# Optimization experiments

Hardware: AMD Instinct MI355X
Metric: run time of the kernel (lower is better)

The kernel has to match this reference:

```python
import jax, jax.numpy as jnp
import numpy as np

E = 8           # num experts
TOPK = 2
NUM_TOKENS = 4096
K = 2048        # hidden dim
N = 2816        # intermediate dim
P = NUM_TOKENS * TOPK   # num_valid_tokens (token, expert-slot) pairs
PE = P // E             # pairs per expert (token-sorted, equal load)


def setup_inputs() -> dict:
    key = jax.random.key(0)
    ks = jax.random.split(key, 6)
    x = jax.random.normal(ks[0], (NUM_TOKENS, K), dtype=jnp.float32)
    W1 = jax.random.normal(ks[1], (E, N, K), dtype=jnp.float32) * (K ** -0.5)  # gate proj
    W3 = jax.random.normal(ks[2], (E, N, K), dtype=jnp.float32) * (K ** -0.5)  # up proj
    W2 = jax.random.normal(ks[3], (E, K, N), dtype=jnp.float32) * (N ** -0.5)  # down proj
    topk_weights = jax.random.uniform(ks[4], (P,), dtype=jnp.float32)          # router weights per pair
    sorted_token_ids = jax.random.randint(ks[5], (P,), 0, NUM_TOKENS, dtype=jnp.int32)
    # token-sorted dispatch: pairs grouped by expert, equal count per expert
    expert_ids = jnp.repeat(jnp.arange(E, dtype=jnp.int32), PE)
    return {"x": x, "W1": W1, "W3": W3, "W2": W2,
            "topk_weights": topk_weights,
            "sorted_token_ids": sorted_token_ids,
            "expert_ids": expert_ids}


def reference(x, W1, W3, W2, topk_weights, sorted_token_ids, expert_ids):
    # Pairs are grouped by expert (token-sorted dispatch), PE pairs per expert.
    eids = expert_ids.reshape(E, PE)[:, 0]            # expert id per group
    xg = x[sorted_token_ids].reshape(E, PE, K)        # gather token activations per pair
    gate = jnp.einsum('epk,enk->epn', xg, W1[eids])   # [E, PE, N]
    up = jnp.einsum('epk,enk->epn', xg, W3[eids])     # [E, PE, N]
    # kernel computes sigmoid(gate) * up (as written in the triton body)
    h = jax.nn.sigmoid(gate) * up
    out_p = jnp.einsum('epn,ekn->epk', h, W2[eids])   # down proj, [E, PE, K]
    out_p = out_p * topk_weights.reshape(E, PE, 1)
    # scatter-add per-pair results into per-token output (atomic_add in kernel)
    out = jnp.zeros((x.shape[0], K), dtype=x.dtype)
    out = out.at[sorted_token_ids].add(out_p.reshape(P, K))
    return out
```

## Files before the change

kernel.cpp:

```cpp
#include <hip/hip_runtime.h>
#include <hip/hip_bf16.h>
#include <cstdint>

typedef __bf16 bf16_t;
typedef __attribute__((ext_vector_type(8))) __bf16 bf16x8;
typedef __attribute__((ext_vector_type(4))) __bf16 bf16x4;
typedef __attribute__((ext_vector_type(4))) float f32x4;

#define NEXP 8
#define NTOK 4096
#define DK   2048
#define DN   2816
#define DN2  5632
#define NP   8192
#define PPE  1024

__global__ void k_convert(const float* __restrict__ src, bf16_t* __restrict__ dst,
                          int perExp4, long dstStride, long dstOff, int total4) {
    int stride = gridDim.x * blockDim.x;
    for (int i = blockIdx.x * blockDim.x + threadIdx.x; i < total4; i += stride) {
        int e  = i / perExp4;
        int r4 = i - e * perExp4;
        float4 v = reinterpret_cast<const float4*>(src)[i];
        bf16x4 o = { (bf16_t)v.x, (bf16_t)v.y, (bf16_t)v.z, (bf16_t)v.w };
        *reinterpret_cast<bf16x4*>(dst + (long)e * dstStride + dstOff + (long)r4 * 4) = o;
    }
}

__global__ void k_gather(const float* __restrict__ x, const int* __restrict__ ids,
                         bf16_t* __restrict__ xg) {
    int i = blockIdx.x * blockDim.x + threadIdx.x;
    if (i >= NP * (DK / 4)) return;
    int p  = i >> 9;
    int c4 = i & 511;
    int tok = ids[p];
    float4 v = reinterpret_cast<const float4*>(x + (size_t)tok * DK)[c4];
    bf16x4 o = { (bf16_t)v.x, (bf16_t)v.y, (bf16_t)v.z, (bf16_t)v.w };
    *reinterpret_cast<bf16x4*>(xg + (size_t)p * DK + c4 * 4) = o;
}

__global__ void k_act(bf16_t* __restrict__ gu) {
    int i = blockIdx.x * blockDim.x + threadIdx.x;
    if (i >= NP * (DN / 8)) return;
    int p = i / (DN / 8);
    int c = i - p * (DN / 8);
    bf16_t* row = gu + (size_t)p * DN2 + c * 8;
    bf16x8 g = *reinterpret_cast<const bf16x8*>(row);
    bf16x8 u = *reinterpret_cast<const bf16x8*>(row + DN);
    bf16x8 h;
#pragma unroll
    for (int j = 0; j < 8; ++j) {
        float gf = (float)g[j], uf = (float)u[j];
        float s = 1.0f / (1.0f + __expf(-gf));
        h[j] = (bf16_t)(s * uf);
    }
    *reinterpret_cast<bf16x8*>(row) = h;
}

__device__ __forceinline__ void gl2lds16(const bf16_t* g, bf16_t* l) {
    __builtin_amdgcn_global_load_lds(
        (__attribute__((address_space(1))) void*)(const_cast<bf16_t*>(g)),
        (__attribute__((address_space(3))) void*)(l), 16, 0, 0);
}

template <int EPI>
__launch_bounds__(256, 2)
__global__ void k_gemm(const bf16_t* __restrict__ A, const bf16_t* __restrict__ B,
                       bf16_t* __restrict__ Cb, float* __restrict__ Cf,
                       const float* __restrict__ tw, const int* __restrict__ ids,
                       int Mtiles, int Ntiles, int Kd, int lda, int ldb,
                       long aStride, long bStride, int ldc, long cStride) {
    __shared__ bf16_t As[128 * 64];
    __shared__ bf16_t Bs[128 * 64];
    const int tpe = Mtiles * Ntiles;
    const int e  = blockIdx.x / tpe;
    const int r  = blockIdx.x - e * tpe;
    const int mt = r / Ntiles;
    const int nt = r - mt * Ntiles;
    const bf16_t* Ae = A + (long)e * aStride + (long)mt * 128 * lda;
    const bf16_t* Be = B + (long)e * bStride + (long)nt * 128 * ldb;
    const int wid  = threadIdx.x >> 6;
    const int lane = threadIdx.x & 63;
    const int wr = wid >> 1, wc = wid & 1;
    const int lr = lane & 15;
    const int lk = (lane >> 4) * 8;
    const int srow = wid * 32 + (lane >> 3);
    const int scol = (lane & 7) * 8;

    f32x4 acc[4][4];
#pragma unroll
    for (int a = 0; a < 4; ++a)
#pragma unroll
        for (int b = 0; b < 4; ++b) acc[a][b] = (f32x4){0.f, 0.f, 0.f, 0.f};

    const int kTiles = Kd >> 6;
    for (int kt = 0; kt < kTiles; ++kt) {
        __syncthreads();
        const bf16_t* ap = Ae + kt * 64 + scol;
        const bf16_t* bp = Be + kt * 64 + scol;
#pragma unroll
        for (int j = 0; j < 4; ++j) {
            gl2lds16(ap + (long)(srow + j * 8) * lda, &As[(wid * 32 + j * 8) * 64]);
            gl2lds16(bp + (long)(srow + j * 8) * ldb, &Bs[(wid * 32 + j * 8) * 64]);
        }
        __syncthreads();
#pragma unroll
        for (int kk = 0; kk < 2; ++kk) {
            bf16x8 af[4], bfr[4];
#pragma unroll
            for (int mi = 0; mi < 4; ++mi)
                af[mi] = *reinterpret_cast<const bf16x8*>(
                    &As[(wr * 64 + mi * 16 + lr) * 64 + kk * 32 + lk]);
#pragma unroll
            for (int ni = 0; ni < 4; ++ni)
                bfr[ni] = *reinterpret_cast<const bf16x8*>(
                    &Bs[(wc * 64 + ni * 16 + lr) * 64 + kk * 32 + lk]);
#pragma unroll
            for (int mi = 0; mi < 4; ++mi)
#pragma unroll
                for (int ni = 0; ni < 4; ++ni)
                    acc[mi][ni] = __builtin_amdgcn_mfma_f32_16x16x32_bf16(
                        af[mi], bfr[ni], acc[mi][ni], 0, 0, 0);
        }
    }

    const int orow0 = wr * 64 + (lane >> 4) * 4;
    const int ocol0 = wc * 64 + (lane & 15);
    if constexpr (EPI == 0) {
        bf16_t* Ce = Cb + (long)e * cStride + (long)mt * 128 * ldc + (long)nt * 128;
#pragma unroll
        for (int mi = 0; mi < 4; ++mi)
#pragma unroll
            for (int i = 0; i < 4; ++i) {
                int row = orow0 + mi * 16 + i;
#pragma unroll
                for (int ni = 0; ni < 4; ++ni)
                    Ce[(long)row * ldc + ocol0 + ni * 16] = (bf16_t)acc[mi][ni][i];
            }
    } else {
        const int p0 = e * PPE + mt * 128;
#pragma unroll
        for (int mi = 0; mi < 4; ++mi)
#pragma unroll
            for (int i = 0; i < 4; ++i) {
                int gp  = p0 + orow0 + mi * 16 + i;
                float w = tw[gp];
                float* orow = Cf + (size_t)ids[gp] * DK + nt * 128 + ocol0;
#pragma unroll
                for (int ni = 0; ni < 4; ++ni)
                    atomicAdd(&orow[ni * 16], acc[mi][ni][i] * w);
            }
    }
}

extern "C" void kernel_launch(void* const* d_in, const int* in_sizes, int n_in,
                              void* d_out, int out_size, void* d_ws, size_t ws_size,
                              hipStream_t stream) {
    const float* x   = (const float*)d_in[0];
    const float* W1  = (const float*)d_in[1];
    const float* W3  = (const float*)d_in[2];
    const float* W2  = (const float*)d_in[3];
    const float* tw  = (const float*)d_in[4];
    const int*   sid = (const int*)d_in[5];
    float* out = (float*)d_out;

    char* ws = (char*)d_ws;
    bf16_t* w13b = (bf16_t*)ws;
    bf16_t* w2b  = (bf16_t*)(ws + 184549376L);
    bf16_t* xg   = (bf16_t*)(ws + 184549376L + 92274688L);
    bf16_t* gu   = (bf16_t*)(ws + 184549376L + 92274688L + 33554432L);

    hipMemsetAsync(d_out, 0, (size_t)out_size * sizeof(float), stream);

    const int per4 = DN * DK / 4;
    const int tot4 = NEXP * per4;
    k_convert<<<2048, 256, 0, stream>>>(W1, w13b, per4, (long)DN2 * DK, 0L, tot4);
    k_convert<<<2048, 256, 0, stream>>>(W3, w13b, per4, (long)DN2 * DK, (long)DN * DK, tot4);
    k_convert<<<2048, 256, 0, stream>>>(W2, w2b, per4, (long)DK * DN, 0L, tot4);
    k_gather<<<NP * (DK / 4) / 256, 256, 0, stream>>>(x, sid, xg);

    k_gemm<0><<<NEXP * 8 * 44, 256, 0, stream>>>(
        xg, w13b, gu, nullptr, nullptr, nullptr,
        8, 44, DK, DK, DK, (long)PPE * DK, (long)DN2 * DK, DN2, (long)PPE * DN2);

    k_act<<<NP * (DN / 8) / 256, 256, 0, stream>>>(gu);

    k_gemm<1><<<NEXP * 8 * 16, 256, 0, stream>>>(
        gu, w2b, nullptr, out, tw, sid,
        8, 16, DN, DN2, DN, (long)PPE * DN2, (long)DK * DN, 0, 0L);
}
```

Baseline: 614.5 us.

## Rewrite MoE GEMMs with 256x256 double-buffered tiles and fused SiLU-style gating epilogue

The GEMM kernel now uses 512-thread blocks with 256x256 tiles, double-buffered LDS with XOR swizzling, interleaved staging and MFMA phases, and setprio hints around the MFMA blocks. W1 and W3 are interleaved in 16-row groups during conversion, so each gate/up pair lands in the same wave. That lets the sigmoid(gate)*up activation be fused into the first GEMM's epilogue, which removes the separate activation kernel and halves the intermediate buffer. The workgroup index is also remapped across expert groups. In exchange there is a much larger register and LDS footprint and many more barriers per k-step.

```diff
diff --git a/kernel.cpp b/kernel.cpp
--- a/kernel.cpp
+++ b/kernel.cpp
@@ -8,22 +8,33 @@
 typedef __attribute__((ext_vector_type(4))) float f32x4;
 
 #define NEXP 8
-#define NTOK 4096
 #define DK   2048
 #define DN   2816
 #define DN2  5632
 #define NP   8192
 #define PPE  1024
 
-__global__ void k_convert(const float* __restrict__ src, bf16_t* __restrict__ dst,
-                          int perExp4, long dstStride, long dstOff, int total4) {
+__global__ void k_cvt(const float* __restrict__ src, bf16_t* __restrict__ dst, int total4) {
     int stride = gridDim.x * blockDim.x;
     for (int i = blockIdx.x * blockDim.x + threadIdx.x; i < total4; i += stride) {
-        int e  = i / perExp4;
-        int r4 = i - e * perExp4;
         float4 v = reinterpret_cast<const float4*>(src)[i];
         bf16x4 o = { (bf16_t)v.x, (bf16_t)v.y, (bf16_t)v.z, (bf16_t)v.w };
-        *reinterpret_cast<bf16x4*>(dst + (long)e * dstStride + dstOff + (long)r4 * 4) = o;
+        reinterpret_cast<bf16x4*>(dst)[i] = o;
+    }
+}
+
+__global__ void k_cvt_w13(const float* __restrict__ src, bf16_t* __restrict__ dst, int rowAdd) {
+    int stride = gridDim.x * blockDim.x;
+    const int total4 = NEXP * DN * (DK / 4);
+    for (int i = blockIdx.x * blockDim.x + threadIdx.x; i < total4; i += stride) {
+        int g  = i >> 9;
+        int c4 = i & 511;
+        int e  = g / DN;
+        int n  = g - e * DN;
+        long drow = (long)e * DN2 + ((n >> 4) << 5) + (n & 15) + rowAdd;
+        float4 v = reinterpret_cast<const float4*>(src)[i];
+        bf16x4 o = { (bf16_t)v.x, (bf16_t)v.y, (bf16_t)v.z, (bf16_t)v.w };
+        *reinterpret_cast<bf16x4*>(dst + drow * DK + c4 * 4) = o;
     }
 }
 
@@ -39,116 +50,175 @@
     *reinterpret_cast<bf16x4*>(xg + (size_t)p * DK + c4 * 4) = o;
 }
 
-__global__ void k_act(bf16_t* __restrict__ gu) {
-    int i = blockIdx.x * blockDim.x + threadIdx.x;
-    if (i >= NP * (DN / 8)) return;
-    int p = i / (DN / 8);
-    int c = i - p * (DN / 8);
-    bf16_t* row = gu + (size_t)p * DN2 + c * 8;
-    bf16x8 g = *reinterpret_cast<const bf16x8*>(row);
-    bf16x8 u = *reinterpret_cast<const bf16x8*>(row + DN);
-    bf16x8 h;
-#pragma unroll
-    for (int j = 0; j < 8; ++j) {
-        float gf = (float)g[j], uf = (float)u[j];
-        float s = 1.0f / (1.0f + __expf(-gf));
-        h[j] = (bf16_t)(s * uf);
-    }
-    *reinterpret_cast<bf16x8*>(row) = h;
-}
-
 __device__ __forceinline__ void gl2lds16(const bf16_t* g, bf16_t* l) {
     __builtin_amdgcn_global_load_lds(
         (__attribute__((address_space(1))) void*)(const_cast<bf16_t*>(g)),
         (__attribute__((address_space(3))) void*)(l), 16, 0, 0);
 }
 
+#define BARX() __builtin_amdgcn_s_barrier()
+#define LGKM0() asm volatile("s_waitcnt lgkmcnt(0)" ::: "memory")
+#define VMW4() asm volatile("s_waitcnt vmcnt(4)" ::: "memory")
+#define VMW0() asm volatile("s_waitcnt vmcnt(0)" ::: "memory")
+
+#define STG(ARR, SRC, LD, BUF, HALF, KT) do {                                   \
+    gl2lds16((SRC) + (long)((HALF) * 128) * (LD) + (long)(KT) * 64,             \
+             &ARR[BUF][(HALF) * 128 + w8][0]);                                  \
+    gl2lds16((SRC) + (long)((HALF) * 128 + 64) * (LD) + (long)(KT) * 64,        \
+             &ARR[BUF][(HALF) * 128 + 64 + w8][0]);                             \
+} while (0)
+
+#define LOADA(DST, BASE) do { _Pragma("unroll")                                 \
+    for (int mi_ = 0; mi_ < 4; ++mi_) {                                         \
+        DST[mi_][0] = *reinterpret_cast<const bf16x8*>((BASE) + aoff0 + mi_ * 1024); \
+        DST[mi_][1] = *reinterpret_cast<const bf16x8*>((BASE) + aoff1 + mi_ * 1024); \
+    } } while (0)
+
+#define LOADB(DST, BASE) do { _Pragma("unroll")                                 \
+    for (int ni_ = 0; ni_ < 2; ++ni_) {                                         \
+        DST[ni_][0] = *reinterpret_cast<const bf16x8*>((BASE) + boff0 + ni_ * 1024); \
+        DST[ni_][1] = *reinterpret_cast<const bf16x8*>((BASE) + boff1 + ni_ * 1024); \
+    } } while (0)
+
+#define MFMAQ(AF, BF, MIB, NIB) do {                                            \
+    __builtin_amdgcn_s_setprio(1);                                              \
+    _Pragma("unroll") for (int kk_ = 0; kk_ < 2; ++kk_)                         \
+    _Pragma("unroll") for (int mi_ = 0; mi_ < 4; ++mi_)                         \
+    _Pragma("unroll") for (int ni_ = 0; ni_ < 2; ++ni_)                         \
+        acc[(MIB) + mi_][(NIB) + ni_] = __builtin_amdgcn_mfma_f32_16x16x32_bf16( \
+            AF[mi_][kk_], BF[ni_][kk_], acc[(MIB) + mi_][(NIB) + ni_], 0, 0, 0); \
+    __builtin_amdgcn_s_setprio(0);                                              \
+} while (0)
+
 template <int EPI>
-__launch_bounds__(256, 2)
+__launch_bounds__(512, 2)
 __global__ void k_gemm(const bf16_t* __restrict__ A, const bf16_t* __restrict__ B,
-                       bf16_t* __restrict__ Cb, float* __restrict__ Cf,
+                       bf16_t* __restrict__ Hout, float* __restrict__ Fout,
                        const float* __restrict__ tw, const int* __restrict__ ids,
-                       int Mtiles, int Ntiles, int Kd, int lda, int ldb,
-                       long aStride, long bStride, int ldc, long cStride) {
-    __shared__ bf16_t As[128 * 64];
-    __shared__ bf16_t Bs[128 * 64];
+                       int Mtiles, int Ntiles, int nkt, int lda, int ldb,
+                       long aStride, long bStride) {
+    __shared__ bf16_t As[2][256][64];
+    __shared__ bf16_t Bs[2][256][64];
+
+    const int nwg = gridDim.x;
+    const int logical = (blockIdx.x & 7) * (nwg >> 3) + (blockIdx.x >> 3);
     const int tpe = Mtiles * Ntiles;
-    const int e  = blockIdx.x / tpe;
-    const int r  = blockIdx.x - e * tpe;
+    const int e  = logical / tpe;
+    const int r  = logical - e * tpe;
     const int mt = r / Ntiles;
     const int nt = r - mt * Ntiles;
-    const bf16_t* Ae = A + (long)e * aStride + (long)mt * 128 * lda;
-    const bf16_t* Be = B + (long)e * bStride + (long)nt * 128 * ldb;
-    const int wid  = threadIdx.x >> 6;
-    const int lane = threadIdx.x & 63;
-    const int wr = wid >> 1, wc = wid & 1;
-    const int lr = lane & 15;
-    const int lk = (lane >> 4) * 8;
-    const int srow = wid * 32 + (lane >> 3);
-    const int scol = (lane & 7) * 8;
-
-    f32x4 acc[4][4];
-#pragma unroll
-    for (int a = 0; a < 4; ++a)
+
+    const int tid  = threadIdx.x;
+    const int w    = tid >> 6;
+    const int w8   = w * 8;
+    const int lane = tid & 63;
+    const int wr = w >> 2, wc = w & 3;
+    const int fr = lane & 15;
+    const int fc = lane >> 4;
+
+    const int srow = tid >> 3;
+    const int schk = (tid & 7) ^ (srow & 7);
+    const bf16_t* aSrc = A + (long)e * aStride + ((long)mt * 256 + srow) * lda + schk * 8;
+    const bf16_t* bSrc = B + (long)e * bStride + ((long)nt * 256 + srow) * ldb + schk * 8;
+
+    const int sx = lane & 7;
+    const int aoff0 = (wr * 128 + fr) * 64 + ((0 + fc) ^ sx) * 8;
+    const int aoff1 = (wr * 128 + fr) * 64 + ((4 + fc) ^ sx) * 8;
+    const int boff0 = (wc * 64 + fr) * 64 + ((0 + fc) ^ sx) * 8;
+    const int boff1 = (wc * 64 + fr) * 64 + ((4 + fc) ^ sx) * 8;
+
+    const bf16_t* As0 = &As[0][0][0];
+    const bf16_t* As1 = &As[1][0][0];
+    const bf16_t* Bs0 = &Bs[0][0][0];
+    const bf16_t* Bs1 = &Bs[1][0][0];
+
+    f32x4 acc[8][4];
+#pragma unroll
+    for (int a = 0; a < 8; ++a)
 #pragma unroll
         for (int b = 0; b < 4; ++b) acc[a][b] = (f32x4){0.f, 0.f, 0.f, 0.f};
 
-    const int kTiles = Kd >> 6;
-    for (int kt = 0; kt < kTiles; ++kt) {
-        __syncthreads();
-        const bf16_t* ap = Ae + kt * 64 + scol;
-        const bf16_t* bp = Be + kt * 64 + scol;
-#pragma unroll
-        for (int j = 0; j < 4; ++j) {
-            gl2lds16(ap + (long)(srow + j * 8) * lda, &As[(wid * 32 + j * 8) * 64]);
-            gl2lds16(bp + (long)(srow + j * 8) * ldb, &Bs[(wid * 32 + j * 8) * 64]);
-        }
-        __syncthreads();
-#pragma unroll
-        for (int kk = 0; kk < 2; ++kk) {
-            bf16x8 af[4], bfr[4];
-#pragma unroll
-            for (int mi = 0; mi < 4; ++mi)
-                af[mi] = *reinterpret_cast<const bf16x8*>(
-                    &As[(wr * 64 + mi * 16 + lr) * 64 + kk * 32 + lk]);
-#pragma unroll
-            for (int ni = 0; ni < 4; ++ni)
-                bfr[ni] = *reinterpret_cast<const bf16x8*>(
-                    &Bs[(wc * 64 + ni * 16 + lr) * 64 + kk * 32 + lk]);
-#pragma unroll
-            for (int mi = 0; mi < 4; ++mi)
-#pragma unroll
-                for (int ni = 0; ni < 4; ++ni)
-                    acc[mi][ni] = __builtin_amdgcn_mfma_f32_16x16x32_bf16(
-                        af[mi], bfr[ni], acc[mi][ni], 0, 0, 0);
-        }
-    }
-
-    const int orow0 = wr * 64 + (lane >> 4) * 4;
-    const int ocol0 = wc * 64 + (lane & 15);
+    bf16x8 af[4][2], ah[4][2], bl[2][2], bh[2][2];
+
+    STG(As, aSrc, lda, 0, 0, 0); STG(As, aSrc, lda, 0, 1, 0);
+    STG(Bs, bSrc, ldb, 0, 0, 0); STG(Bs, bSrc, ldb, 0, 1, 0);
+    STG(Bs, bSrc, ldb, 1, 0, 1); STG(Bs, bSrc, ldb, 1, 1, 1);
+    VMW4();
+    BARX();
+
+    const int nIter = nkt >> 1;
+    for (int it = 0; it < nIter; ++it) {
+        const int t = it * 2;
+        const bool last = (it == nIter - 1);
+        LOADA(af, As0); LOADB(bl, Bs0);
+        STG(As, aSrc, lda, 1, 0, t + 1);
+        BARX(); LGKM0();
+        MFMAQ(af, bl, 0, 0);
+        BARX();
+        LOADB(bh, Bs0 + 2048);
+        STG(As, aSrc, lda, 1, 1, t + 1);
+        BARX(); LGKM0();
+        MFMAQ(af, bh, 0, 2);
+        BARX();
+        LOADA(ah, As0 + 4096);
+        if (!last) STG(Bs, bSrc, ldb, 0, 0, t + 2);
+        BARX(); LGKM0();
+        MFMAQ(ah, bh, 4, 2);
+        BARX();
+        if (!last) { STG(Bs, bSrc, ldb, 0, 1, t + 2); VMW4(); } else { VMW0(); }
+        BARX();
+        MFMAQ(ah, bl, 4, 0);
+        BARX();
+        LOADA(af, As1); LOADB(bl, Bs1);
+        if (!last) STG(As, aSrc, lda, 0, 0, t + 2);
+        BARX(); LGKM0();
+        MFMAQ(af, bl, 0, 0);
+        BARX();
+        LOADB(bh, Bs1 + 2048);
+        if (!last) STG(As, aSrc, lda, 0, 1, t + 2);
+        BARX(); LGKM0();
+        MFMAQ(af, bh, 0, 2);
+        BARX();
+        LOADA(ah, As1 + 4096);
+        if (!last) STG(Bs, bSrc, ldb, 1, 0, t + 3);
+        BARX(); LGKM0();
+        MFMAQ(ah, bh, 4, 2);
+        BARX();
+        if (!last) { STG(Bs, bSrc, ldb, 1, 1, t + 3); VMW4(); } else { VMW0(); }
+        BARX();
+        MFMAQ(ah, bl, 4, 0);
+        BARX();
+    }
+
     if constexpr (EPI == 0) {
-        bf16_t* Ce = Cb + (long)e * cStride + (long)mt * 128 * ldc + (long)nt * 128;
-#pragma unroll
-        for (int mi = 0; mi < 4; ++mi)
+        const long prow0 = (long)e * PPE + (long)mt * 256 + wr * 128 + fc * 4;
+        const int col0 = nt * 128 + wc * 32 + fr;
+#pragma unroll
+        for (int mi = 0; mi < 8; ++mi)
 #pragma unroll
             for (int i = 0; i < 4; ++i) {
-                int row = orow0 + mi * 16 + i;
-#pragma unroll
-                for (int ni = 0; ni < 4; ++ni)
-                    Ce[(long)row * ldc + ocol0 + ni * 16] = (bf16_t)acc[mi][ni][i];
+                long row = prow0 + mi * 16 + i;
+#pragma unroll
+                for (int p = 0; p < 2; ++p) {
+                    float g = acc[mi][2 * p][i];
+                    float u = acc[mi][2 * p + 1][i];
+                    float s = 1.f / (1.f + __expf(-g));
+                    Hout[row * DN + col0 + p * 16] = (bf16_t)(s * u);
+                }
             }
     } else {
-        const int p0 = e * PPE + mt * 128;
-#pragma unroll
-        for (int mi = 0; mi < 4; ++mi)
+        const int p0 = e * PPE + mt * 256 + wr * 128 + fc * 4;
+        const int col0 = nt * 256 + wc * 64 + fr;
+#pragma unroll
+        for (int mi = 0; mi < 8; ++mi)
 #pragma unroll
             for (int i = 0; i < 4; ++i) {
-                int gp  = p0 + orow0 + mi * 16 + i;
-                float w = tw[gp];
-                float* orow = Cf + (size_t)ids[gp] * DK + nt * 128 + ocol0;
+                int gp = p0 + mi * 16 + i;
+                float wgt = tw[gp];
+                float* ob = Fout + (long)ids[gp] * DK + col0;
 #pragma unroll
                 for (int ni = 0; ni < 4; ++ni)
-                    atomicAdd(&orow[ni * 16], acc[mi][ni][i] * w);
+                    atomicAdd(ob + ni * 16, acc[mi][ni][i] * wgt);
             }
     }
 }
@@ -165,27 +235,23 @@
     float* out = (float*)d_out;
 
     char* ws = (char*)d_ws;
-    bf16_t* w13b = (bf16_t*)ws;
+    bf16_t* w13i = (bf16_t*)ws;
     bf16_t* w2b  = (bf16_t*)(ws + 184549376L);
-    bf16_t* xg   = (bf16_t*)(ws + 184549376L + 92274688L);
-    bf16_t* gu   = (bf16_t*)(ws + 184549376L + 92274688L + 33554432L);
+    bf16_t* xg   = (bf16_t*)(ws + 276824064L);
+    bf16_t* h    = (bf16_t*)(ws + 310378496L);
 
     hipMemsetAsync(d_out, 0, (size_t)out_size * sizeof(float), stream);
 
-    const int per4 = DN * DK / 4;
-    const int tot4 = NEXP * per4;
-    k_convert<<<2048, 256, 0, stream>>>(W1, w13b, per4, (long)DN2 * DK, 0L, tot4);
-    k_convert<<<2048, 256, 0, stream>>>(W3, w13b, per4, (long)DN2 * DK, (long)DN * DK, tot4);
-    k_convert<<<2048, 256, 0, stream>>>(W2, w2b, per4, (long)DK * DN, 0L, tot4);
+    k_cvt_w13<<<2048, 256, 0, stream>>>(W1, w13i, 0);
+    k_cvt_w13<<<2048, 256, 0, stream>>>(W3, w13i, 16);
+    k_cvt<<<2048, 256, 0, stream>>>(W2, w2b, NEXP * DK * (DN / 4));
     k_gather<<<NP * (DK / 4) / 256, 256, 0, stream>>>(x, sid, xg);
 
-    k_gemm<0><<<NEXP * 8 * 44, 256, 0, stream>>>(
-        xg, w13b, gu, nullptr, nullptr, nullptr,
-        8, 44, DK, DK, DK, (long)PPE * DK, (long)DN2 * DK, DN2, (long)PPE * DN2);
-
-    k_act<<<NP * (DN / 8) / 256, 256, 0, stream>>>(gu);
-
-    k_gemm<1><<<NEXP * 8 * 16, 256, 0, stream>>>(
-        gu, w2b, nullptr, out, tw, sid,
-        8, 16, DN, DN2, DN, (long)PPE * DN2, (long)DK * DN, 0, 0L);
-}
+    k_gemm<0><<<NEXP * 4 * 22, 512, 0, stream>>>(
+        xg, w13i, h, nullptr, nullptr, nullptr,
+        4, 22, 32, DK, DK, (long)PPE * DK, (long)DN2 * DK);
+
+    k_gemm<1><<<NEXP * 4 * 8, 512, 0, stream>>>(
+        h, w2b, nullptr, out, tw, sid,
+        4, 8, 44, DN, DN, (long)PPE * DN, (long)DK * DN);
+}
```

After: 507.8 us. 1.21x faster.
